# Kernel optimization log

Measured on AMD Instinct MI355X. Metric: run time of the kernel, lower is better.

Reference implementation:

```python
import jax, jax.numpy as jnp
import numpy as np

# HyenaConfig constants (match init_kwargs)
SEQ_LEN = 8192
HIDDEN_DIM = 768
EMB_DIM = 3
FILTER_ORDER = 64
FAST_DECAY_PCT = 0.3
SLOW_DECAY_PCT = 1.5
TARGET = 0.01
SHIFT = 0.0


def setup_inputs() -> dict:
    key = jax.random.key(0)
    ks = jax.random.split(key, 9)
    return {
        "x": jax.random.normal(ks[0], (8, SEQ_LEN, HIDDEN_DIM), dtype=jnp.float32),
        "w_in": jax.random.normal(ks[1], (EMB_DIM, FILTER_ORDER), dtype=jnp.float32),
        "b_in": jax.random.normal(ks[2], (FILTER_ORDER,), dtype=jnp.float32),
        "freq_in": jnp.ones((1, FILTER_ORDER), dtype=jnp.float32),
        "w_h0": jax.random.normal(ks[3], (FILTER_ORDER, FILTER_ORDER), dtype=jnp.float32),
        "b_h0": jax.random.normal(ks[4], (FILTER_ORDER,), dtype=jnp.float32),
        "freq_h0": jnp.ones((1, FILTER_ORDER), dtype=jnp.float32),
        "w_h1": jax.random.normal(ks[5], (FILTER_ORDER, FILTER_ORDER), dtype=jnp.float32),
        "b_h1": jax.random.normal(ks[6], (FILTER_ORDER,), dtype=jnp.float32),
        "freq_h1": jnp.ones((1, FILTER_ORDER), dtype=jnp.float32),
        "w_out": jax.random.normal(ks[7], (FILTER_ORDER, HIDDEN_DIM), dtype=jnp.float32),
        "bias": jax.random.normal(ks[8], (HIDDEN_DIM,), dtype=jnp.float32),
        "L": SEQ_LEN,
    }


def _pos_emb(L):
    # PositionalEmbedding.init: t in [0,1], z = [t, Re(e^{-i f w}), Im(e^{-i f w})]
    t = jnp.linspace(0.0, 1.0, L, dtype=jnp.float32).reshape(L, 1)
    bands = (EMB_DIM - 1) // 2
    t_rescaled = jnp.linspace(0.0, L - 1, L, dtype=jnp.float32).reshape(L, 1)
    w = 2.0 * jnp.pi * t_rescaled / L  # (L, 1)
    f = jnp.linspace(1e-4, bands - 1, bands, dtype=jnp.float32).reshape(1, bands)
    phase = f * w  # (L, bands)
    z = jnp.concatenate([t, jnp.cos(phase), -jnp.sin(phase)], axis=-1)  # (L, EMB_DIM)
    return z, t


def _filter_k(L, w_in, b_in, freq_in, w_h0, b_h0, freq_h0, w_h1, b_h1, freq_h1, w_out):
    z, t = _pos_emb(L)
    # ImplicitFilterMLP: Linear -> Sin -> (Linear -> Sin) x2 -> Linear (no bias)
    h = jnp.sin(freq_in * (z @ w_in + b_in))
    h = jnp.sin(freq_h0 * (h @ w_h0 + b_h0))
    h = jnp.sin(freq_h1 * (h @ w_h1 + b_h1))
    h = h @ w_out  # (L, HIDDEN_DIM)
    # ExponentialModulation
    max_decay = jnp.log(TARGET) / FAST_DECAY_PCT
    min_decay = jnp.log(TARGET) / SLOW_DECAY_PCT
    deltas = jnp.linspace(min_decay, max_decay, HIDDEN_DIM, dtype=jnp.float32)  # (D,)
    decay = jnp.exp(-t * jnp.abs(deltas))  # (L, D)
    return h * (decay + SHIFT)


def _fft_conv(u, k, bias):
    # u: (B, L, D), k: (L, D)
    seqlen = u.shape[-2]
    fft_size = 2 * seqlen
    u_f = jnp.fft.rfft(u, n=fft_size, axis=-2)
    k_f = jnp.fft.rfft(k[None], n=fft_size, axis=-2) / fft_size
    y = jnp.fft.irfft(u_f * k_f, n=fft_size, axis=-2)[..., :seqlen, :]
    return y + bias.reshape(1, 1, -1)


def reference(x, w_in, b_in, freq_in, w_h0, b_h0, freq_h0, w_h1, b_h1, freq_h1,
              w_out, bias, L):
    k = _filter_k(L, w_in, b_in, freq_in, w_h0, b_h0, freq_h0, w_h1, b_h1,
                  freq_h1, w_out)  # (L, D)
    return _fft_conv(x, k, bias)
```

## Files before the change

kernel.cpp:

```cpp
#include <hip/hip_runtime.h>
#include <stdint.h>

typedef __bf16   bf16x8 __attribute__((ext_vector_type(8)));
typedef float    f32x4  __attribute__((ext_vector_type(4)));
typedef uint32_t u32x4  __attribute__((ext_vector_type(4)));

#define L_SEQ 8192
#define DIM   768
#define DROW  8768


__global__ __launch_bounds__(256) void pad_kernel(uint32_t* __restrict__ dupG)
{
  int d = blockIdx.x;
  const int NPAD = 31 + (DROW - 8224);
  for (int j = threadIdx.x; j < NPAD; j += 256) {
    int i = (j < 31) ? j : 8224 + (j - 31);
    dupG[(size_t)d * DROW + i] = 0u;
  }
}

__global__ __launch_bounds__(256) void filter_kernel(
    const float* __restrict__ w_in, const float* __restrict__ b_in,
    const float* __restrict__ freq_in,
    const float* __restrict__ w_h0, const float* __restrict__ b_h0,
    const float* __restrict__ freq_h0,
    const float* __restrict__ w_h1, const float* __restrict__ b_h1,
    const float* __restrict__ freq_h1,
    const float* __restrict__ w_out,
    uint32_t* __restrict__ dupG)
{
  __shared__ float h1[33][65];
  __shared__ float h2[33][65];
  __shared__ unsigned short kv[33][64];
  __shared__ float wch[64][64];

  const int c = blockIdx.x;
  const int sbase = c << 5;
  const int tid = threadIdx.x;

  for (int p = tid; p < 33 * 64; p += 256) {
    int j = p >> 6, n = p & 63;
    int s = sbase - 1 + j;
    float t  = s * (1.0f / 8191.0f);
    float ph = s * (float)(6.283185307179586 * 1e-4 / 8192.0);
    float a = t * w_in[n] + cosf(ph) * w_in[64 + n] + (-sinf(ph)) * w_in[128 + n] + b_in[n];
    h1[j][n] = sinf(freq_in[n] * a);
  }
  __syncthreads();
  for (int p = tid; p < 33 * 64; p += 256) {
    int j = p >> 6, n = p & 63;
    float a = b_h0[n];
    for (int r = 0; r < 64; ++r) a += h1[j][r] * w_h0[r * 64 + n];
    h2[j][n] = sinf(freq_h0[n] * a);
  }
  __syncthreads();
  for (int p = tid; p < 33 * 64; p += 256) {
    int j = p >> 6, n = p & 63;
    float a = b_h1[n];
    for (int r = 0; r < 64; ++r) a += h2[j][r] * w_h1[r * 64 + n];
    h1[j][n] = sinf(freq_h1[n] * a);
  }
  __syncthreads();

  for (int dc = 0; dc < 12; ++dc) {
    for (int p = tid; p < 64 * 64; p += 256) {
      int r = p >> 6, dd = p & 63;
      wch[r][dd] = w_out[r * DIM + dc * 64 + dd];
    }
    __syncthreads();
    for (int p = tid; p < 33 * 64; p += 256) {
      int j = p >> 6, dd = p & 63;
      float a = 0.0f;
      for (int r = 0; r < 64; ++r) a += h1[j][r] * wch[r][dd];
      int s = sbase - 1 + j;
      int d = dc * 64 + dd;
      float delta = fabsf(-3.070113457f - 12.280453827f * (d * (1.0f / 767.0f)));
      float t = s * (1.0f / 8191.0f);
      float val = (s < 0) ? 0.0f : a * expf(-t * delta) * 6.103515625e-05f;
      kv[j][dd] = __builtin_bit_cast(unsigned short, (__bf16)val);
    }
    __syncthreads();
    for (int p = tid; p < 32 * 64; p += 256) {
      int j = p >> 6, dd = p & 63;
      int d = dc * 64 + dd;
      int i = 8223 - (sbase + j);
      dupG[(size_t)d * DROW + i] =
          (uint32_t)kv[j + 1][dd] | ((uint32_t)kv[j][dd] << 16);
    }
    if (c == 255 && tid < 64) {
      int d = dc * 64 + tid;
      dupG[(size_t)d * DROW + 31] = ((uint32_t)kv[32][tid] << 16);
    }
    __syncthreads();
  }
}

__global__ __launch_bounds__(256) void transpose_in_kernel(
    const float* __restrict__ x, unsigned short* __restrict__ uT)
{
  __shared__ unsigned short tile[64][66];
  int b = blockIdx.z;
  int t0 = blockIdx.y * 64;
  int d0 = blockIdx.x * 64;
  int tid = threadIdx.x;
  int j = tid & 63, i0 = tid >> 6;
  for (int ii = 0; ii < 16; ++ii) {
    int tt = i0 * 16 + ii;
    float v = x[((size_t)b * L_SEQ + t0 + tt) * DIM + d0 + j];
    tile[tt][j] = __builtin_bit_cast(unsigned short, (__bf16)v);
  }
  __syncthreads();
  for (int ii = 0; ii < 16; ++ii) {
    int dd = i0 + ii * 4;
    uT[((size_t)(d0 + dd) * 8 + b) * L_SEQ + t0 + j] = tile[j][dd];
  }
}

#define LOADFRAG(dst, absdw) {                                    \
    int _p = ((absdw) & 2047);                                    \
    u32x4 _u = { buf[_p], buf[_p + 2], buf[_p + 4], buf[_p + 6] };\
    dst = __builtin_bit_cast(bf16x8, _u); }

__global__ __launch_bounds__(256) void conv_kernel(
    const uint32_t* __restrict__ dupG,
    const unsigned short* __restrict__ uT,
    unsigned short* __restrict__ yT)
{
  const int d   = blockIdx.y;
  const int T0  = blockIdx.x << 10;
  const int tid = threadIdx.x;
  const int lane = tid & 63;
  const int w    = tid >> 6;
  const int m = lane & 15, q = lane >> 4;
  const int h = (lane >> 3) & 1;
  __shared__ uint32_t buf[2080];

  f32x4 acc[8] = {};
  bf16x8 fr2[8];
  bf16x8 zfr = {};

  float delta = fabsf(-3.070113457f - 12.280453827f * (d * (1.0f / 767.0f)));
  int S = (int)(8191.0f * 3.5065578f / delta);
  int tau_start = T0 - S;
  tau_start = (tau_start < 0) ? 0 : (tau_start & ~31);
  int niter = ((T0 + 992 - tau_start) >> 5) + 1;
  niter = (niter + 7) & ~7;

  const uint32_t* dG = dupG + (size_t)d * DROW;
  const unsigned short* uTd = uT + ((size_t)d << 16);

  int i0 = 7200 + tau_start - T0;

  for (int j = tid; j < 1280; j += 256) {
    int i = i0 + j;
    uint32_t v = dG[i];
    int pos = i & 2047;
    buf[pos] = v;
    if (pos < 32) buf[2048 + pos] = v;
  }
  __syncthreads();

  int a_off = ((lane & 7) << 14) + ((tau_start - 16 + (h << 4) + (q << 3)) << 1);
  int vb = i0 + 1007 - (w << 8) - m + (q << 3);
  int chunk_i = i0 + 1280;

  const bool kill = (tau_start == 0) & (h == 0) & (q < 2);

  LOADFRAG(fr2[7], vb - 32);
  LOADFRAG(fr2[6], vb - 64);
  LOADFRAG(fr2[5], vb - 96);
  LOADFRAG(fr2[4], vb - 128);
  LOADFRAG(fr2[3], vb - 160);
  LOADFRAG(fr2[2], vb - 192);
  LOADFRAG(fr2[1], vb - 224);

#define MFMA_J(rr, j)                                                          \
  acc[j] = __builtin_amdgcn_mfma_f32_16x16x32_bf16(                            \
      afrag, fr2[((rr) - (j)) & 7], acc[j], 0, 0, 0);

#define BODY(rr, K0) {                                                         \
    bf16x8 afrag = *(const bf16x8*)((const char*)uTd + a_off + ((rr) << 6));   \
    if (K0) { if (kill) afrag = zfr; }                                         \
    LOADFRAG(fr2[(rr) & 7], vb + ((rr) << 5));                                 \
    MFMA_J(rr, 1) MFMA_J(rr, 2) MFMA_J(rr, 3) MFMA_J(rr, 4)                    \
    MFMA_J(rr, 5) MFMA_J(rr, 6) MFMA_J(rr, 7) MFMA_J(rr, 0)                    \
  }

  {
    int si = chunk_i + tid;
    int iv = (si < 8744) ? si : 8744;
    uint32_t stage = dG[iv];
    BODY(0, 1) BODY(1, 0) BODY(2, 0) BODY(3, 0)
    BODY(4, 0) BODY(5, 0) BODY(6, 0) BODY(7, 0)
    int pos = si & 2047;
    buf[pos] = stage;
    if (pos < 32) buf[2048 + pos] = stage;
    __syncthreads();
    a_off += 512; vb += 256; chunk_i += 256;
  }
  for (int nn = 8; nn < niter; nn += 8) {
    int si = chunk_i + tid;
    int iv = (si < 8744) ? si : 8744;
    uint32_t stage = dG[iv];
    BODY(0, 0) BODY(1, 0) BODY(2, 0) BODY(3, 0)
    BODY(4, 0) BODY(5, 0) BODY(6, 0) BODY(7, 0)
    int pos = si & 2047;
    buf[pos] = stage;
    if (pos < 32) buf[2048 + pos] = stage;
    __syncthreads();
    a_off += 512; vb += 256; chunk_i += 256;
  }

#pragma unroll
  for (int j = 0; j < 8; ++j) {
    int tb_ = T0 + (w << 8) + (j << 5) + m;
#pragma unroll
    for (int r = 0; r < 4; ++r) {
      int row = q * 4 + r;
      int bb = row & 7;
      int hh = row >> 3;
      yT[((size_t)(d * 8 + bb) << 13) + tb_ + (hh << 4)] =
          __builtin_bit_cast(unsigned short, (__bf16)acc[j][r]);
    }
  }
}

__global__ __launch_bounds__(256) void transpose_out_kernel(
    const unsigned short* __restrict__ yT, const float* __restrict__ bias,
    float* __restrict__ out)
{
  __shared__ float tile[64][65];
  int b = blockIdx.z;
  int t0 = blockIdx.y * 64;
  int d0 = blockIdx.x * 64;
  int tid = threadIdx.x;
  int j = tid & 63, i0 = tid >> 6;
  for (int ii = 0; ii < 16; ++ii) {
    int dd = i0 * 16 + ii;
    unsigned short v = yT[((size_t)(d0 + dd) * 8 + b) * L_SEQ + t0 + j];
    tile[dd][j] = (float)__builtin_bit_cast(__bf16, v);
  }
  __syncthreads();
  float bs = bias[d0 + j];
  for (int ii = 0; ii < 16; ++ii) {
    int tt = i0 + ii * 4;
    out[((size_t)b * L_SEQ + t0 + tt) * DIM + d0 + j] = tile[j][tt] + bs;
  }
}

extern "C" void kernel_launch(void* const* d_in, const int* in_sizes, int n_in,
                              void* d_out, int out_size, void* d_ws, size_t ws_size,
                              hipStream_t stream)
{
  const float* x       = (const float*)d_in[0];
  const float* w_in    = (const float*)d_in[1];
  const float* b_in    = (const float*)d_in[2];
  const float* freq_in = (const float*)d_in[3];
  const float* w_h0    = (const float*)d_in[4];
  const float* b_h0    = (const float*)d_in[5];
  const float* freq_h0 = (const float*)d_in[6];
  const float* w_h1    = (const float*)d_in[7];
  const float* b_h1    = (const float*)d_in[8];
  const float* freq_h1 = (const float*)d_in[9];
  const float* w_out   = (const float*)d_in[10];
  const float* bias    = (const float*)d_in[11];

  char* ws = (char*)d_ws;
  uint32_t* dupG = (uint32_t*)(ws);
  unsigned short* uT = (unsigned short*)(ws + 26935296);
  unsigned short* yT = (unsigned short*)(ws + 127598592);
  float* out = (float*)d_out;

  hipLaunchKernelGGL(pad_kernel, dim3(DIM), dim3(256), 0, stream, dupG);
  hipLaunchKernelGGL(filter_kernel, dim3(256), dim3(256), 0, stream,
                     w_in, b_in, freq_in, w_h0, b_h0, freq_h0,
                     w_h1, b_h1, freq_h1, w_out, dupG);
  hipLaunchKernelGGL(transpose_in_kernel, dim3(12, 128, 8), dim3(256), 0, stream, x, uT);
  hipLaunchKernelGGL(conv_kernel, dim3(8, DIM), dim3(256), 0, stream, dupG, uT, yT);
  hipLaunchKernelGGL(transpose_out_kernel, dim3(12, 128, 8), dim3(256), 0, stream,
                     yT, bias, out);
}
```

Measured before the change: 933.1 us.

## Vectorize transposes, prefetch A fragments in conv, stage MLP weights in LDS

The input and output transpose kernels now move data with 16-byte global loads and stores, and the output tile holds bf16 instead of float. The conv kernel double-buffers its A-operand fragments in registers, fetching one iteration ahead, and refills the LDS filter window with vector loads from 64 threads. The filter MLP stages w_h0 and w_h1 in shared memory instead of reading them from global memory in the inner loop. The aim is to reduce memory transaction count and latency stalls, at the cost of more registers in the conv kernel and some LDS bank conflicts in the strided tile reads.

```diff
diff --git a/kernel.cpp b/kernel.cpp
--- a/kernel.cpp
+++ b/kernel.cpp
@@ -4,6 +4,8 @@
 typedef __bf16   bf16x8 __attribute__((ext_vector_type(8)));
 typedef float    f32x4  __attribute__((ext_vector_type(4)));
 typedef uint32_t u32x4  __attribute__((ext_vector_type(4)));
+typedef uint32_t u32x2  __attribute__((ext_vector_type(2)));
+typedef unsigned short u16x8 __attribute__((ext_vector_type(8)));
 
 #define L_SEQ 8192
 #define DIM   768
@@ -47,18 +49,21 @@
     float a = t * w_in[n] + cosf(ph) * w_in[64 + n] + (-sinf(ph)) * w_in[128 + n] + b_in[n];
     h1[j][n] = sinf(freq_in[n] * a);
   }
+  for (int p = tid; p < 64 * 64; p += 256) wch[p >> 6][p & 63] = w_h0[p];
   __syncthreads();
   for (int p = tid; p < 33 * 64; p += 256) {
     int j = p >> 6, n = p & 63;
     float a = b_h0[n];
-    for (int r = 0; r < 64; ++r) a += h1[j][r] * w_h0[r * 64 + n];
+    for (int r = 0; r < 64; ++r) a += h1[j][r] * wch[r][n];
     h2[j][n] = sinf(freq_h0[n] * a);
   }
+  __syncthreads();
+  for (int p = tid; p < 64 * 64; p += 256) wch[p >> 6][p & 63] = w_h1[p];
   __syncthreads();
   for (int p = tid; p < 33 * 64; p += 256) {
     int j = p >> 6, n = p & 63;
     float a = b_h1[n];
-    for (int r = 0; r < 64; ++r) a += h2[j][r] * w_h1[r * 64 + n];
+    for (int r = 0; r < 64; ++r) a += h2[j][r] * wch[r][n];
     h1[j][n] = sinf(freq_h1[n] * a);
   }
   __syncthreads();
@@ -99,21 +104,37 @@
 __global__ __launch_bounds__(256) void transpose_in_kernel(
     const float* __restrict__ x, unsigned short* __restrict__ uT)
 {
-  __shared__ unsigned short tile[64][66];
+  __shared__ unsigned short tile[64][68];
   int b = blockIdx.z;
   int t0 = blockIdx.y * 64;
   int d0 = blockIdx.x * 64;
   int tid = threadIdx.x;
-  int j = tid & 63, i0 = tid >> 6;
-  for (int ii = 0; ii < 16; ++ii) {
-    int tt = i0 * 16 + ii;
-    float v = x[((size_t)b * L_SEQ + t0 + tt) * DIM + d0 + j];
-    tile[tt][j] = __builtin_bit_cast(unsigned short, (__bf16)v);
-  }
-  __syncthreads();
-  for (int ii = 0; ii < 16; ++ii) {
-    int dd = i0 + ii * 4;
-    uT[((size_t)(d0 + dd) * 8 + b) * L_SEQ + t0 + j] = tile[j][dd];
+
+  int ld = tid & 15;
+  int tq = tid >> 4;
+#pragma unroll
+  for (int it = 0; it < 4; ++it) {
+    int trow = tq + 16 * it;
+    f32x4 xv = *(const f32x4*)&x[((size_t)b * L_SEQ + t0 + trow) * DIM + d0 + 4 * ld];
+    unsigned short s0 = __builtin_bit_cast(unsigned short, (__bf16)xv[0]);
+    unsigned short s1 = __builtin_bit_cast(unsigned short, (__bf16)xv[1]);
+    unsigned short s2 = __builtin_bit_cast(unsigned short, (__bf16)xv[2]);
+    unsigned short s3 = __builtin_bit_cast(unsigned short, (__bf16)xv[3]);
+    u32x2 pk = { (uint32_t)s0 | ((uint32_t)s1 << 16),
+                 (uint32_t)s2 | ((uint32_t)s3 << 16) };
+    *(u32x2*)&tile[trow][4 * ld] = pk;
+  }
+  __syncthreads();
+
+  int l = tid & 63, w = tid >> 6;
+  int toct = l & 7;
+#pragma unroll
+  for (int it = 0; it < 2; ++it) {
+    int d = 8 * w + 32 * it + (l >> 3);
+    u16x8 o;
+#pragma unroll
+    for (int c2 = 0; c2 < 8; ++c2) o[c2] = tile[8 * toct + c2][d];
+    *(u16x8*)&uT[((size_t)(d0 + d) * 8 + b) * L_SEQ + t0 + 8 * toct] = o;
   }
 }
 
@@ -138,6 +159,7 @@
 
   f32x4 acc[8] = {};
   bf16x8 fr2[8];
+  bf16x8 pa[8];
   bf16x8 zfr = {};
 
   float delta = fabsf(-3.070113457f - 12.280453827f * (d * (1.0f / 767.0f)));
@@ -152,20 +174,26 @@
 
   int i0 = 7200 + tau_start - T0;
 
-  for (int j = tid; j < 1280; j += 256) {
-    int i = i0 + j;
-    uint32_t v = dG[i];
+  int a_off = ((lane & 7) << 14) + ((tau_start - 16 + (h << 4) + (q << 3)) << 1);
+
+#pragma unroll
+  for (int rr = 0; rr < 8; ++rr)
+    pa[rr] = *(const bf16x8*)((const char*)uTd + a_off + (rr << 6));
+
+  for (int j4 = tid * 4; j4 < 1280; j4 += 1024) {
+    int i = i0 + j4;
+    u32x4 v = *(const u32x4*)&dG[i];
     int pos = i & 2047;
-    buf[pos] = v;
-    if (pos < 32) buf[2048 + pos] = v;
-  }
-  __syncthreads();
-
-  int a_off = ((lane & 7) << 14) + ((tau_start - 16 + (h << 4) + (q << 3)) << 1);
+    *(u32x4*)&buf[pos] = v;
+    if (pos < 32) *(u32x4*)&buf[2048 + pos] = v;
+  }
+  __syncthreads();
+
+  const bool kill = (tau_start == 0) & (h == 0) & (q < 2);
+  if (kill) pa[0] = zfr;
+
   int vb = i0 + 1007 - (w << 8) - m + (q << 3);
   int chunk_i = i0 + 1280;
-
-  const bool kill = (tau_start == 0) & (h == 0) & (q < 2);
 
   LOADFRAG(fr2[7], vb - 32);
   LOADFRAG(fr2[6], vb - 64);
@@ -179,35 +207,28 @@
   acc[j] = __builtin_amdgcn_mfma_f32_16x16x32_bf16(                            \
       afrag, fr2[((rr) - (j)) & 7], acc[j], 0, 0, 0);
 
-#define BODY(rr, K0) {                                                         \
-    bf16x8 afrag = *(const bf16x8*)((const char*)uTd + a_off + ((rr) << 6));   \
-    if (K0) { if (kill) afrag = zfr; }                                         \
+#define BODY(rr) {                                                             \
     LOADFRAG(fr2[(rr) & 7], vb + ((rr) << 5));                                 \
+    bf16x8 afrag = pa[rr];                                                     \
+    pa[rr] = *(const bf16x8*)((const char*)uTd + a_off + ((rr) << 6) + 512);   \
     MFMA_J(rr, 1) MFMA_J(rr, 2) MFMA_J(rr, 3) MFMA_J(rr, 4)                    \
     MFMA_J(rr, 5) MFMA_J(rr, 6) MFMA_J(rr, 7) MFMA_J(rr, 0)                    \
   }
 
-  {
-    int si = chunk_i + tid;
-    int iv = (si < 8744) ? si : 8744;
-    uint32_t stage = dG[iv];
-    BODY(0, 1) BODY(1, 0) BODY(2, 0) BODY(3, 0)
-    BODY(4, 0) BODY(5, 0) BODY(6, 0) BODY(7, 0)
-    int pos = si & 2047;
-    buf[pos] = stage;
-    if (pos < 32) buf[2048 + pos] = stage;
-    __syncthreads();
-    a_off += 512; vb += 256; chunk_i += 256;
-  }
-  for (int nn = 8; nn < niter; nn += 8) {
-    int si = chunk_i + tid;
-    int iv = (si < 8744) ? si : 8744;
-    uint32_t stage = dG[iv];
-    BODY(0, 0) BODY(1, 0) BODY(2, 0) BODY(3, 0)
-    BODY(4, 0) BODY(5, 0) BODY(6, 0) BODY(7, 0)
-    int pos = si & 2047;
-    buf[pos] = stage;
-    if (pos < 32) buf[2048 + pos] = stage;
+  for (int nn = 0; nn < niter; nn += 8) {
+    u32x4 stage = {};
+    int si4 = chunk_i + (tid << 2);
+    if (tid < 64) {
+      int iv = (si4 < 8740) ? si4 : 8740;
+      stage = *(const u32x4*)&dG[iv];
+    }
+    BODY(0) BODY(1) BODY(2) BODY(3)
+    BODY(4) BODY(5) BODY(6) BODY(7)
+    if (tid < 64) {
+      int pos = si4 & 2047;
+      *(u32x4*)&buf[pos] = stage;
+      if (pos < 32) *(u32x4*)&buf[2048 + pos] = stage;
+    }
     __syncthreads();
     a_off += 512; vb += 256; chunk_i += 256;
   }
@@ -230,22 +251,36 @@
     const unsigned short* __restrict__ yT, const float* __restrict__ bias,
     float* __restrict__ out)
 {
-  __shared__ float tile[64][65];
+  __shared__ unsigned short tile[64][68];
   int b = blockIdx.z;
   int t0 = blockIdx.y * 64;
   int d0 = blockIdx.x * 64;
   int tid = threadIdx.x;
-  int j = tid & 63, i0 = tid >> 6;
-  for (int ii = 0; ii < 16; ++ii) {
-    int dd = i0 * 16 + ii;
-    unsigned short v = yT[((size_t)(d0 + dd) * 8 + b) * L_SEQ + t0 + j];
-    tile[dd][j] = (float)__builtin_bit_cast(__bf16, v);
-  }
-  __syncthreads();
-  float bs = bias[d0 + j];
-  for (int ii = 0; ii < 16; ++ii) {
-    int tt = i0 + ii * 4;
-    out[((size_t)b * L_SEQ + t0 + tt) * DIM + d0 + j] = tile[j][tt] + bs;
+
+  int l = tid & 63, w = tid >> 6;
+  int toct = l & 7;
+#pragma unroll
+  for (int it = 0; it < 2; ++it) {
+    int d = 8 * w + 32 * it + (l >> 3);
+    u16x8 o = *(const u16x8*)&yT[((size_t)(d0 + d) * 8 + b) * L_SEQ + t0 + 8 * toct];
+#pragma unroll
+    for (int c2 = 0; c2 < 8; ++c2) tile[8 * toct + c2][d] = o[c2];
+  }
+  __syncthreads();
+
+  int ld = tid & 15;
+  int tq = tid >> 4;
+  f32x4 bs = *(const f32x4*)&bias[d0 + 4 * ld];
+#pragma unroll
+  for (int it = 0; it < 4; ++it) {
+    int trow = tq + 16 * it;
+    u32x2 pk = *(const u32x2*)&tile[trow][4 * ld];
+    f32x4 ov;
+    ov[0] = (float)__builtin_bit_cast(__bf16, (unsigned short)(pk[0] & 0xffff)) + bs[0];
+    ov[1] = (float)__builtin_bit_cast(__bf16, (unsigned short)(pk[0] >> 16))    + bs[1];
+    ov[2] = (float)__builtin_bit_cast(__bf16, (unsigned short)(pk[1] & 0xffff)) + bs[2];
+    ov[3] = (float)__builtin_bit_cast(__bf16, (unsigned short)(pk[1] >> 16))    + bs[3];
+    *(f32x4*)&out[((size_t)b * L_SEQ + t0 + trow) * DIM + d0 + 4 * ld] = ov;
   }
 }
 
```

After: 941.7 us. Within noise of the previous version (+0.9%).
